# Performance work log

Measured on AMD Instinct MI355X. Metric: run time of the kernel, lower is better.

Reference implementation:

```python
import jax, jax.numpy as jnp
import numpy as np

NEG = -1e30  # finite stand-in for -inf in the sparse-softmax mask


def setup_inputs() -> dict:
    key = jax.random.key(0)
    kh, kwl, kwn, kn = jax.random.split(key, 4)
    B, S, D, E = 8, 4096, 1024, 64
    return {
        "h": jax.random.normal(kh, (B, S, D), dtype=jnp.float32),
        "Wl": jax.random.normal(kwl, (E, D), dtype=jnp.float32) * 0.02,
        "bl": jnp.zeros((E,), dtype=jnp.float32),
        "Wn": jax.random.normal(kwn, (E, D), dtype=jnp.float32) * 0.02,
        "bn": jnp.zeros((E,), dtype=jnp.float32),
        "noise": jax.random.normal(kn, (B, S, E), dtype=jnp.float32),
        "top_k": 2,
    }


def reference(h, Wl, bl, Wn, bn, noise, top_k):
    # logits, noise std: two small linears over the expert dim
    logits = jnp.einsum("bsd,ed->bse", h, Wl) + bl          # [B,S,E]
    std = jax.nn.softplus(jnp.einsum("bsd,ed->bse", h, Wn) + bn)
    noisy = logits + noise * std                              # [B,S,E]

    full_p = jax.nn.softmax(noisy, axis=-1)

    topk_vals, ix = jax.lax.top_k(noisy, top_k)               # [B,S,k]
    E = noisy.shape[-1]
    # scatter top-k values back into a -inf-filled tensor == mask non-topk
    mask = jax.nn.one_hot(ix, E, dtype=jnp.bool_).any(axis=-2)  # [B,S,E]
    sparse = jnp.where(mask, noisy, NEG)
    route_p = jax.nn.softmax(sparse, axis=-1)
    return route_p, ix, full_p
```

## Files before the change

kernel.cpp:

```cpp
#include <hip/hip_runtime.h>
#include <math.h>


#define DIM 1024
#define NEXP 64
#define LS 40
#define CS 132
#define HALF_BUF 15360
#define A_LO 2560
#define B_HI 5120
#define B_LO 10240
#define LOSCALE 2048.0f
#define INV_LOSCALE (1.0f / 2048.0f)

using half4v   = __attribute__((ext_vector_type(4)))  _Float16;
using half8v   = __attribute__((ext_vector_type(8)))  _Float16;
using floatx16 = __attribute__((ext_vector_type(16))) float;

__device__ inline void split4(const float4 v, half4v& hi, half4v& lo) {
    _Float16 h0 = (_Float16)v.x, h1 = (_Float16)v.y,
             h2 = (_Float16)v.z, h3 = (_Float16)v.w;
    hi = (half4v){h0, h1, h2, h3};
    lo = (half4v){(_Float16)((v.x - (float)h0) * LOSCALE),
                  (_Float16)((v.y - (float)h1) * LOSCALE),
                  (_Float16)((v.z - (float)h2) * LOSCALE),
                  (_Float16)((v.w - (float)h3) * LOSCALE)};
}

#define MFMA32(a, b, c) __builtin_amdgcn_mfma_f32_32x32x16_f16((a), (b), (c), 0, 0, 0)

__global__ __launch_bounds__(512, 4)
void router_fused(const float* __restrict__ h,  const float* __restrict__ Wl,
                  const float* __restrict__ bl, const float* __restrict__ Wn,
                  const float* __restrict__ bn, const float* __restrict__ noise,
                  float* __restrict__ outR, float* __restrict__ outIx,
                  float* __restrict__ outF, int M)
{
    __shared__ _Float16 lds[2 * HALF_BUF];

    const int tid   = threadIdx.x;
    const int wv    = tid >> 6;
    const int lane  = tid & 63;
    const int row31 = lane & 31;
    const int oct   = lane >> 5;
    const int tokg  = (wv >> 2) * 32;
    const int expg  = (wv & 3) * 32;
    const int tok0  = blockIdx.x * 64;

    const int srow = tid >> 3;
    const int skq  = tid & 7;
    const float* hp  = h  + (size_t)(tok0 + srow) * DIM + skq * 4;
    const float* wp0 = Wl + (size_t)srow * DIM + skq * 4;
    const float* wp1 = Wn + (size_t)srow * DIM + skq * 4;
    const int sA  = srow * LS + skq * 4;
    const int sB0 = B_HI + srow * LS + skq * 4;
    const int sB1 = B_HI + (srow + 64) * LS + skq * 4;

    const int aoffs = (tokg + row31) * LS + oct * 8;
    const int boffs = (expg + row31) * LS + oct * 8;

    floatx16 acc1, acc2;
#pragma unroll
    for (int i = 0; i < 16; i++) { acc1[i] = 0.f; acc2[i] = 0.f; }

    float4 av  = *(const float4*)(hp);
    float4 bv0 = *(const float4*)(wp0);
    float4 bv1 = *(const float4*)(wp1);
    {
        half4v hi, lo;
        split4(av, hi, lo);
        *(half4v*)(lds + sA) = hi;        *(half4v*)(lds + A_LO + sA) = lo;
        split4(bv0, hi, lo);
        *(half4v*)(lds + sB0) = hi;       *(half4v*)(lds + B_LO - B_HI + sB0) = lo;
        split4(bv1, hi, lo);
        *(half4v*)(lds + sB1) = hi;       *(half4v*)(lds + B_LO - B_HI + sB1) = lo;
    }
    av  = *(const float4*)(hp + 32);
    bv0 = *(const float4*)(wp0 + 32);
    bv1 = *(const float4*)(wp1 + 32);
    __syncthreads();

    for (int t = 0; t < 32; t++) {
        if (t < 31) {
            _Float16* bufS = lds + ((t + 1) & 1) * HALF_BUF;
            half4v hi, lo;
            split4(av, hi, lo);
            *(half4v*)(bufS + sA) = hi;   *(half4v*)(bufS + A_LO + sA) = lo;
            split4(bv0, hi, lo);
            *(half4v*)(bufS + sB0) = hi;  *(half4v*)(bufS + B_LO - B_HI + sB0) = lo;
            split4(bv1, hi, lo);
            *(half4v*)(bufS + sB1) = hi;  *(half4v*)(bufS + B_LO - B_HI + sB1) = lo;
        }
        if (t < 30) {
            av  = *(const float4*)(hp  + 32 * (t + 2));
            bv0 = *(const float4*)(wp0 + 32 * (t + 2));
            bv1 = *(const float4*)(wp1 + 32 * (t + 2));
        }
        {
            const _Float16* bufC = lds + (t & 1) * HALF_BUF;
#pragma unroll
            for (int ks = 0; ks < 2; ks++) {
                half8v aH = *(const half8v*)(bufC + aoffs + ks * 16);
                half8v aL = *(const half8v*)(bufC + A_LO + aoffs + ks * 16);
                half8v bH = *(const half8v*)(bufC + B_HI + boffs + ks * 16);
                half8v bL = *(const half8v*)(bufC + B_LO + boffs + ks * 16);
                acc1 = MFMA32(aH, bH, acc1);
                acc2 = MFMA32(aH, bL, acc2);
                acc2 = MFMA32(aL, bH, acc2);
            }
        }
        __syncthreads();
    }

    float* Cs = (float*)lds;
#pragma unroll
    for (int i = 0; i < 16; i++) {
        int rowt = (i & 3) + 8 * (i >> 2) + 4 * oct;
        Cs[(tokg + rowt) * CS + expg + row31] = acc1[i] + acc2[i] * INV_LOSCALE;
    }
    __syncthreads();

    const float blv = bl[lane];
    const float bnv = bn[lane];

    for (int t = wv; t < 64; t += 8) {
        const int gt = tok0 + t;
        float xr = Cs[t * CS + lane] + blv;
        float xf = Cs[t * CS + 64 + lane] + bnv;
        float nz = noise[(size_t)gt * NEXP + lane];

        float stdv = fmaxf(xf, 0.f) + log1pf(expf(-fabsf(xf)));
        float noisy = fmaf(nz, stdv, xr);

        float m = noisy;
#pragma unroll
        for (int o = 32; o > 0; o >>= 1) m = fmaxf(m, __shfl_xor(m, o, 64));
        float p = expf(noisy - m);
        float s = p;
#pragma unroll
        for (int o = 32; o > 0; o >>= 1) s += __shfl_xor(s, o, 64);
        float fullp = p / s;

        float v = noisy; int idx = lane;
#pragma unroll
        for (int o = 32; o > 0; o >>= 1) {
            float ov = __shfl_xor(v, o, 64);
            int   oi = __shfl_xor(idx, o, 64);
            if (ov > v || (ov == v && oi < idx)) { v = ov; idx = oi; }
        }
        const float v1 = v; const int i1 = idx;
        v = (lane == i1) ? -INFINITY : noisy; idx = lane;
#pragma unroll
        for (int o = 32; o > 0; o >>= 1) {
            float ov = __shfl_xor(v, o, 64);
            int   oi = __shfl_xor(idx, o, 64);
            if (ov > v || (ov == v && oi < idx)) { v = ov; idx = oi; }
        }
        const float v2 = v; const int i2 = idx;

        float e2 = expf(v2 - v1);
        float den = 1.f + e2;
        float routep = (lane == i1) ? (1.f / den) : ((lane == i2) ? (e2 / den) : 0.f);

        outR[(size_t)gt * NEXP + lane] = routep;
        outF[(size_t)gt * NEXP + lane] = fullp;
        if (lane == 0) {
            outIx[(size_t)gt * 2 + 0] = (float)i1;
            outIx[(size_t)gt * 2 + 1] = (float)i2;
        }
    }
}

extern "C" void kernel_launch(void* const* d_in, const int* in_sizes, int n_in,
                              void* d_out, int out_size, void* d_ws, size_t ws_size,
                              hipStream_t stream) {
    const float* h     = (const float*)d_in[0];
    const float* Wl    = (const float*)d_in[1];
    const float* bl    = (const float*)d_in[2];
    const float* Wn    = (const float*)d_in[3];
    const float* bn    = (const float*)d_in[4];
    const float* noise = (const float*)d_in[5];
    float* out = (float*)d_out;

    const int M = in_sizes[0] / DIM;
    float* outR  = out;
    float* outIx = out + (size_t)M * NEXP;
    float* outF  = outIx + (size_t)M * 2;

    router_fused<<<M / 64, 512, 0, stream>>>(h, Wl, bl, Wn, bn, noise,
                                             outR, outIx, outF, M);
}
```

Before: 238.8 us.

## Pre-split weights once and stream tiles into LDS with direct global-to-LDS loads

Adds a prep kernel that converts both weight matrices once into swizzled fp16 hi/lo tiles in workspace. The main kernel now loads the activation and weight tiles directly into LDS with global_load_lds and an XOR swizzle, and does the activation hi/lo split when reading from LDS. This removes per-block weight conversion and register staging of the global loads. It adds a second launch and relies on the barrier to wait for the asynchronous LDS loads.

Result: no change. 243.6 us (+2.0%).

```diff
diff --git a/kernel.cpp b/kernel.cpp
--- a/kernel.cpp
+++ b/kernel.cpp
@@ -4,39 +4,53 @@
 
 #define DIM 1024
 #define NEXP 64
-#define LS 40
 #define CS 132
-#define HALF_BUF 15360
-#define A_LO 2560
-#define B_HI 5120
-#define B_LO 10240
 #define LOSCALE 2048.0f
 #define INV_LOSCALE (1.0f / 2048.0f)
 
-using half4v   = __attribute__((ext_vector_type(4)))  _Float16;
 using half8v   = __attribute__((ext_vector_type(8)))  _Float16;
 using floatx16 = __attribute__((ext_vector_type(16))) float;
 
-__device__ inline void split4(const float4 v, half4v& hi, half4v& lo) {
-    _Float16 h0 = (_Float16)v.x, h1 = (_Float16)v.y,
-             h2 = (_Float16)v.z, h3 = (_Float16)v.w;
-    hi = (half4v){h0, h1, h2, h3};
-    lo = (half4v){(_Float16)((v.x - (float)h0) * LOSCALE),
-                  (_Float16)((v.y - (float)h1) * LOSCALE),
-                  (_Float16)((v.z - (float)h2) * LOSCALE),
-                  (_Float16)((v.w - (float)h3) * LOSCALE)};
-}
-
 #define MFMA32(a, b, c) __builtin_amdgcn_mfma_f32_32x32x16_f16((a), (b), (c), 0, 0, 0)
 
+__device__ inline void gll16(const void* g, void* l) {
+    __builtin_amdgcn_global_load_lds(
+        (const __attribute__((address_space(1))) unsigned int*)g,
+        (__attribute__((address_space(3))) unsigned int*)l, 16, 0, 0);
+}
+
+__global__ __launch_bounds__(512)
+void prep_B(const float* __restrict__ Wl, const float* __restrict__ Wn,
+            _Float16* __restrict__ Bp)
+{
+    const int idx = blockIdx.x * 512 + threadIdx.x;
+    const int r  = idx >> 7;
+    const int c2 = idx & 127;
+    const float* W = (r < 64) ? (Wl + (size_t)r * DIM) : (Wn + (size_t)(r - 64) * DIM);
+    float f[8];
+    *(float4*)(f)     = *(const float4*)(W + c2 * 8);
+    *(float4*)(f + 4) = *(const float4*)(W + c2 * 8 + 4);
+    half8v hi, lo;
+#pragma unroll
+    for (int i = 0; i < 8; i++) {
+        _Float16 hh = (_Float16)f[i];
+        hi[i] = hh;
+        lo[i] = (_Float16)((f[i] - (float)hh) * LOSCALE);
+    }
+    const int t = c2 >> 2, cf = c2 & 3, sw = r & 7;
+    _Float16* base = Bp + ((size_t)t * 128 + r) * 64;
+    *(half8v*)(base + ((cf ^ sw) << 3))      = hi;
+    *(half8v*)(base + (((4 | cf) ^ sw) << 3)) = lo;
+}
+
 __global__ __launch_bounds__(512, 4)
-void router_fused(const float* __restrict__ h,  const float* __restrict__ Wl,
-                  const float* __restrict__ bl, const float* __restrict__ Wn,
-                  const float* __restrict__ bn, const float* __restrict__ noise,
+void router_fused(const float* __restrict__ h, const _Float16* __restrict__ Bp,
+                  const float* __restrict__ bl, const float* __restrict__ bn,
+                  const float* __restrict__ noise,
                   float* __restrict__ outR, float* __restrict__ outIx,
-                  float* __restrict__ outF, int M)
+                  float* __restrict__ outF)
 {
-    __shared__ _Float16 lds[2 * HALF_BUF];
+    __shared__ __align__(16) char lds_raw[49152];
 
     const int tid   = threadIdx.x;
     const int wv    = tid >> 6;
@@ -47,72 +61,65 @@
     const int expg  = (wv & 3) * 32;
     const int tok0  = blockIdx.x * 64;
 
-    const int srow = tid >> 3;
-    const int skq  = tid & 7;
-    const float* hp  = h  + (size_t)(tok0 + srow) * DIM + skq * 4;
-    const float* wp0 = Wl + (size_t)srow * DIM + skq * 4;
-    const float* wp1 = Wn + (size_t)srow * DIM + skq * 4;
-    const int sA  = srow * LS + skq * 4;
-    const int sB0 = B_HI + srow * LS + skq * 4;
-    const int sB1 = B_HI + (srow + 64) * LS + skq * 4;
-
-    const int aoffs = (tokg + row31) * LS + oct * 8;
-    const int boffs = (expg + row31) * LS + oct * 8;
+    const int rS = tid >> 3, cS = tid & 7;
+    const float*    aSrc = h + (size_t)(tok0 + rS) * DIM + ((cS ^ (rS & 7)) << 2);
+    const _Float16* bSrc = Bp + (size_t)tid * 8;
+    char* dA = lds_raw + (tid << 4);
+    char* dB = lds_raw + 16384 + (tid << 4);
+
+#define ISSUE(tt, sel) do { \
+        gll16(aSrc + (tt) * 32,                  dA + (sel) * 8192);        \
+        gll16(bSrc + (size_t)(tt) * 8192,        dB + (sel) * 16384);       \
+        gll16(bSrc + (size_t)(tt) * 8192 + 4096, dB + (sel) * 16384 + 8192);\
+    } while (0)
+
+    const int rA = tokg + row31, rB = expg + row31;
+    const int swA = (rA & 7) << 4, swB = (rB & 7) << 4;
+    const char* A0p = lds_raw + rA * 128;
+    const char* A1p = A0p + 8192;
+    const char* B0p = lds_raw + 16384 + rB * 128;
+    const char* B1p = B0p + 16384;
+    const int a00 = (oct * 32) ^ swA,      a01 = (oct * 32 + 16) ^ swA;
+    const int a10 = (64 + oct * 32) ^ swA, a11 = (64 + oct * 32 + 16) ^ swA;
+    const int bh0 = (oct * 16) ^ swB,      bh1 = (32 + oct * 16) ^ swB;
+    const int bl0 = (64 + oct * 16) ^ swB, bl1 = (96 + oct * 16) ^ swB;
 
     floatx16 acc1, acc2;
 #pragma unroll
     for (int i = 0; i < 16; i++) { acc1[i] = 0.f; acc2[i] = 0.f; }
 
-    float4 av  = *(const float4*)(hp);
-    float4 bv0 = *(const float4*)(wp0);
-    float4 bv1 = *(const float4*)(wp1);
-    {
-        half4v hi, lo;
-        split4(av, hi, lo);
-        *(half4v*)(lds + sA) = hi;        *(half4v*)(lds + A_LO + sA) = lo;
-        split4(bv0, hi, lo);
-        *(half4v*)(lds + sB0) = hi;       *(half4v*)(lds + B_LO - B_HI + sB0) = lo;
-        split4(bv1, hi, lo);
-        *(half4v*)(lds + sB1) = hi;       *(half4v*)(lds + B_LO - B_HI + sB1) = lo;
-    }
-    av  = *(const float4*)(hp + 32);
-    bv0 = *(const float4*)(wp0 + 32);
-    bv1 = *(const float4*)(wp1 + 32);
+    ISSUE(0, 0);
+    ISSUE(1, 1);
     __syncthreads();
 
+#pragma unroll 2
     for (int t = 0; t < 32; t++) {
-        if (t < 31) {
-            _Float16* bufS = lds + ((t + 1) & 1) * HALF_BUF;
-            half4v hi, lo;
-            split4(av, hi, lo);
-            *(half4v*)(bufS + sA) = hi;   *(half4v*)(bufS + A_LO + sA) = lo;
-            split4(bv0, hi, lo);
-            *(half4v*)(bufS + sB0) = hi;  *(half4v*)(bufS + B_LO - B_HI + sB0) = lo;
-            split4(bv1, hi, lo);
-            *(half4v*)(bufS + sB1) = hi;  *(half4v*)(bufS + B_LO - B_HI + sB1) = lo;
-        }
-        if (t < 30) {
-            av  = *(const float4*)(hp  + 32 * (t + 2));
-            bv0 = *(const float4*)(wp0 + 32 * (t + 2));
-            bv1 = *(const float4*)(wp1 + 32 * (t + 2));
-        }
-        {
-            const _Float16* bufC = lds + (t & 1) * HALF_BUF;
-#pragma unroll
-            for (int ks = 0; ks < 2; ks++) {
-                half8v aH = *(const half8v*)(bufC + aoffs + ks * 16);
-                half8v aL = *(const half8v*)(bufC + A_LO + aoffs + ks * 16);
-                half8v bH = *(const half8v*)(bufC + B_HI + boffs + ks * 16);
-                half8v bL = *(const half8v*)(bufC + B_LO + boffs + ks * 16);
-                acc1 = MFMA32(aH, bH, acc1);
-                acc2 = MFMA32(aH, bL, acc2);
-                acc2 = MFMA32(aL, bH, acc2);
+        const char* Ab = (t & 1) ? A1p : A0p;
+        const char* Bb = (t & 1) ? B1p : B0p;
+#pragma unroll
+        for (int ks = 0; ks < 2; ks++) {
+            const float4 f0 = *(const float4*)(Ab + (ks ? a10 : a00));
+            const float4 f1 = *(const float4*)(Ab + (ks ? a11 : a01));
+            const half8v bH = *(const half8v*)(Bb + (ks ? bh1 : bh0));
+            const half8v bL = *(const half8v*)(Bb + (ks ? bl1 : bl0));
+            float f[8] = {f0.x, f0.y, f0.z, f0.w, f1.x, f1.y, f1.z, f1.w};
+            half8v aH, aL;
+#pragma unroll
+            for (int i = 0; i < 8; i++) {
+                _Float16 hh = (_Float16)f[i];
+                aH[i] = hh;
+                aL[i] = (_Float16)((f[i] - (float)hh) * LOSCALE);
             }
+            acc1 = MFMA32(aH, bH, acc1);
+            acc2 = MFMA32(aH, bL, acc2);
+            acc2 = MFMA32(aL, bH, acc2);
         }
         __syncthreads();
-    }
-
-    float* Cs = (float*)lds;
+        if (t < 30) ISSUE(t + 2, t & 1);
+    }
+#undef ISSUE
+
+    float* Cs = (float*)lds_raw;
 #pragma unroll
     for (int i = 0; i < 16; i++) {
         int rowt = (i & 3) + 8 * (i >> 2) + 4 * oct;
@@ -187,6 +194,8 @@
     float* outIx = out + (size_t)M * NEXP;
     float* outF  = outIx + (size_t)M * 2;
 
-    router_fused<<<M / 64, 512, 0, stream>>>(h, Wl, bl, Wn, bn, noise,
-                                             outR, outIx, outF, M);
-}
+    _Float16* Bp = (_Float16*)d_ws;
+
+    prep_B<<<32, 512, 0, stream>>>(Wl, Wn, Bp);
+    router_fused<<<M / 64, 512, 0, stream>>>(h, Bp, bl, bn, noise, outR, outIx, outF);
+}
```
